# Optimization experiments

Hardware: AMD Instinct MI355X
Metric: run time of the kernel (lower is better)

## Reference

```python
import jax, jax.numpy as jnp
import numpy as np

B, N, F_IN, F_OUT = 8, 2048, 256, 256
H, D = 8, 32
LN_EPS = 1e-5


def setup_inputs() -> dict:
    key = jax.random.key(0)
    ks = jax.random.split(key, 8)
    s = 1.0 / np.sqrt(F_IN)
    so = 1.0 / np.sqrt(H * D)
    return {
        "x": jax.random.normal(ks[0], (B, N, F_IN), dtype=jnp.float32),
        "adj": jax.random.randint(ks[1], (B, N, N), 0, 2, dtype=jnp.int32),
        "Wq": jax.random.uniform(ks[2], (F_IN, H * D), jnp.float32, -s, s),
        "bq": jnp.zeros((H * D,), jnp.float32),
        "Wk": jax.random.uniform(ks[3], (F_IN, H * D), jnp.float32, -s, s),
        "bk": jnp.zeros((H * D,), jnp.float32),
        "Wv": jax.random.uniform(ks[4], (F_IN, H * D), jnp.float32, -s, s),
        "bv": jnp.zeros((H * D,), jnp.float32),
        "Wo": jax.random.uniform(ks[5], (H * D, F_OUT), jnp.float32, -so, so),
        "bo": jnp.zeros((F_OUT,), jnp.float32),
        "gamma": jnp.ones((F_OUT,), jnp.float32),
        "beta": jnp.zeros((F_OUT,), jnp.float32),
    }


def reference(x, adj, Wq, bq, Wk, bk, Wv, bv, Wo, bo, gamma, beta):
    b, n, _ = x.shape
    # QKV projections -> [B, H, N, D]
    q = (x @ Wq + bq).reshape(b, n, H, D).transpose(0, 2, 1, 3)
    k = (x @ Wk + bk).reshape(b, n, H, D).transpose(0, 2, 1, 3)
    v = (x @ Wv + bv).reshape(b, n, H, D).transpose(0, 2, 1, 3)
    # masked attention scores [B, H, N, N]
    scores = jnp.einsum('bhqd,bhkd->bhqk', q, k) / np.sqrt(D).astype(np.float32)
    scores = jnp.where(adj[:, None, :, :] == 0, -jnp.inf, scores)
    attn = jax.nn.softmax(scores, axis=-1)
    # dropout layers are identity in eval mode
    out = jnp.einsum('bhqk,bhkd->bhqd', attn, v)
    out = out.transpose(0, 2, 1, 3).reshape(b, n, H * D)
    out = out @ Wo + bo
    # LayerNorm
    mu = out.mean(-1, keepdims=True)
    var = out.var(-1, keepdims=True)
    out = (out - mu) * jax.lax.rsqrt(var + LN_EPS) * gamma + beta
    return out, attn.mean(axis=1)
```

## Files before the change

### kernel.cpp

```cpp
#include <hip/hip_runtime.h>


typedef __attribute__((ext_vector_type(8))) short short8;
typedef __attribute__((ext_vector_type(4))) float f32x4;
typedef __attribute__((ext_vector_type(4))) unsigned short us4;
typedef unsigned short u16;
typedef unsigned int u32;

#define SC2 0.25503486127240555f

__device__ __forceinline__ u16 cvt(float f) {
  __bf16 h = (__bf16)f;
  union { __bf16 h; u16 u; } v; v.h = h; return v.u;
}

__global__ __launch_bounds__(256) void k_prep(
    const int* __restrict__ adj, u32* __restrict__ packed,
    const float* __restrict__ w0, const float* __restrict__ w1,
    const float* __restrict__ w2, const float* __restrict__ w3,
    u16* __restrict__ o0, u16* __restrict__ o1,
    u16* __restrict__ o2, u16* __restrict__ o3) {
  int bid = blockIdx.x;
  if (bid < 256) {
    int z = bid >> 6, rem = bid & 63;
    const float* in; u16* out;
    if (z == 0) { in = w0; out = o0; }
    else if (z == 1) { in = w1; out = o1; }
    else if (z == 2) { in = w2; out = o2; }
    else { in = w3; out = o3; }
    __shared__ u16 t[32][33];
    int tx = threadIdx.x & 31, ty = threadIdx.x >> 5;
    int x0 = (rem & 7) * 32, y0 = (rem >> 3) * 32;
    for (int j = 0; j < 32; j += 8)
      t[ty + j][tx] = cvt(in[(y0 + ty + j) * 256 + x0 + tx]);
    __syncthreads();
    for (int j = 0; j < 32; j += 8)
      out[(x0 + ty + j) * 256 + y0 + tx] = t[tx][ty + j];
  } else {
    int lane = threadIdx.x & 63;
#pragma unroll 4
    for (int it = 0; it < 64; it++) {
      unsigned int i = ((bid - 256) * 64u + it) * 256u + threadIdx.x;
      unsigned long long m = __ballot(adj[i] != 0);
      if (lane == 0)       packed[i >> 5] = (u32)m;
      else if (lane == 32) packed[i >> 5] = (u32)(m >> 32);
    }
  }
}

__global__ __launch_bounds__(256) void k_qkv(
    const float* __restrict__ x, const u16* __restrict__ wt,
    const float* __restrict__ bq, const float* __restrict__ bk,
    const float* __restrict__ bv,
    u16* __restrict__ qw, u16* __restrict__ kw, u16* __restrict__ vt) {
  int l = threadIdx.x & 63, w = threadIdx.x >> 6;
  int lr = l & 15, lg = l >> 4;
  int row0 = blockIdx.y * 64 + w * 16;
  int c0 = blockIdx.x * 64;
  f32x4 acc[4] = {};
  const float* xr = x + (size_t)(row0 + lr) * 256 + lg * 8;
  const u16* wr = wt + (c0 + lr) * 256 + lg * 8;
  for (int k0 = 0; k0 < 256; k0 += 32) {
    f32x4 f0 = *(const f32x4*)(xr + k0);
    f32x4 f1 = *(const f32x4*)(xr + k0 + 4);
    short8 a;
    a[0] = (short)cvt(f0[0]); a[1] = (short)cvt(f0[1]);
    a[2] = (short)cvt(f0[2]); a[3] = (short)cvt(f0[3]);
    a[4] = (short)cvt(f1[0]); a[5] = (short)cvt(f1[1]);
    a[6] = (short)cvt(f1[2]); a[7] = (short)cvt(f1[3]);
#pragma unroll
    for (int ct = 0; ct < 4; ct++) {
      short8 bb = *(const short8*)(wr + ct * 16 * 256 + k0);
      acc[ct] = __builtin_amdgcn_mfma_f32_16x16x32_bf16(a, bb, acc[ct], 0, 0, 0);
    }
  }
  int mtx = blockIdx.x >> 2;
  const float* bias = (mtx == 0) ? bq : ((mtx == 1) ? bk : bv);
  int b = row0 >> 11, nbase = row0 & 2047;
#pragma unroll
  for (int ct = 0; ct < 4; ct++) {
    int cc = (c0 + ct * 16 + lr) & 255;
    int h = cc >> 5, d = cc & 31;
    float bs = bias[cc];
    if (mtx < 2) {
      u16* dst = (mtx == 0) ? qw : kw;
      float sc = (mtx == 0) ? SC2 : 1.0f;
#pragma unroll
      for (int rr = 0; rr < 4; rr++) {
        int n = nbase + lg * 4 + rr;
        dst[((b * 8 + h) * 2048 + n) * 32 + d] = cvt((acc[ct][rr] + bs) * sc);
      }
    } else {
      us4 pk;
#pragma unroll
      for (int rr = 0; rr < 4; rr++) pk[rr] = cvt(acc[ct][rr] + bs);
      *(us4*)(vt + (size_t)((b * 8 + h) * 32 + d) * 2048 + nbase + lg * 4) = pk;
    }
  }
}

__global__ __launch_bounds__(512) void k_attn(
    const u16* __restrict__ qw, const u16* __restrict__ kw,
    const u16* __restrict__ vt, const u32* __restrict__ packed,
    u16* __restrict__ ao, float* __restrict__ out2) {
  __shared__ __align__(16) u16 P[8][2048];
  __shared__ float lsbuf[8][32];
  int l = threadIdx.x & 63, wv = threadIdx.x >> 6;
  int lr = l & 15, lg = l >> 4;
  int b = blockIdx.y, q0 = blockIdx.x * 32;
  const u32* pkb = packed + (size_t)(b * 2048 + q0) * 64;

  {
    int h = wv;
    const u16* qb = qw + (size_t)((b * 8 + h) * 2048 + q0) * 32;
    const u16* kb = kw + (size_t)((b * 8 + h) * 2048) * 32;
    const u16* vb = vt + (size_t)((b * 8 + h) * 32) * 2048;
    short8 qf0 = *(const short8*)(qb + lr * 32 + lg * 8);
    short8 qf1 = *(const short8*)(qb + (16 + lr) * 32 + lg * 8);
    u16* Pt = &P[h][0];
    float ls0 = 0.f, ls1 = 0.f;
    f32x4 acc[2][2] = {};
    for (int ch = 0; ch < 32; ch++) {
      uint2 m0 = *(const uint2*)(pkb + lr * 64 + ch * 2);
      uint2 m1 = *(const uint2*)(pkb + (16 + lr) * 64 + ch * 2);
#pragma unroll
      for (int j = 0; j < 4; j++) {
        short8 kf = *(const short8*)(kb + (size_t)(ch * 64 + j * 16 + lr) * 32 + lg * 8);
        f32x4 z = {};
        f32x4 s0 = __builtin_amdgcn_mfma_f32_16x16x32_bf16(kf, qf0, z, 0, 0, 0);
        f32x4 s1 = __builtin_amdgcn_mfma_f32_16x16x32_bf16(kf, qf1, z, 0, 0, 0);
        u32 w0 = ((j & 2) ? m0.y : m0.x) >> ((j & 1) * 16 + lg * 4);
        u32 w1 = ((j & 2) ? m1.y : m1.x) >> ((j & 1) * 16 + lg * 4);
        us4 p0, p1;
#pragma unroll
        for (int rr = 0; rr < 4; rr++) {
          float e0 = __builtin_exp2f(s0[rr]);
          float e1 = __builtin_exp2f(s1[rr]);
          float em0 = ((w0 >> rr) & 1u) ? e0 : 0.0f;
          float em1 = ((w1 >> rr) & 1u) ? e1 : 0.0f;
          ls0 += em0; ls1 += em1;
          p0[rr] = cvt(em0); p1[rr] = cvt(em1);
        }
        int slot = 2 * j + (lg >> 1), offs = (lg & 1) * 4;
        *(us4*)(Pt + lr * 64 + ((slot ^ (lr & 7)) << 3) + offs) = p0;
        *(us4*)(Pt + (16 + lr) * 64 + ((slot ^ (lr & 7)) << 3) + offs) = p1;
      }
#pragma unroll
      for (int k2 = 0; k2 < 2; k2++) {
        short8 pa0 = *(const short8*)(Pt + lr * 64 +
                        (((k2 * 4 + lg) ^ (lr & 7)) << 3));
        short8 pa1 = *(const short8*)(Pt + (16 + lr) * 64 +
                        (((k2 * 4 + lg) ^ (lr & 7)) << 3));
#pragma unroll
        for (int dt = 0; dt < 2; dt++) {
          short8 vf = *(const short8*)(vb + (size_t)(dt * 16 + lr) * 2048 +
                                       ch * 64 + k2 * 32 + lg * 8);
          acc[0][dt] = __builtin_amdgcn_mfma_f32_16x16x32_bf16(pa0, vf, acc[0][dt], 0, 0, 0);
          acc[1][dt] = __builtin_amdgcn_mfma_f32_16x16x32_bf16(pa1, vf, acc[1][dt], 0, 0, 0);
        }
      }
    }
    ls0 += __shfl_xor(ls0, 16); ls0 += __shfl_xor(ls0, 32);
    ls1 += __shfl_xor(ls1, 16); ls1 += __shfl_xor(ls1, 32);
    ls0 = fmaxf(ls0, 1e-30f); ls1 = fmaxf(ls1, 1e-30f);
    if (l < 16) { lsbuf[h][lr] = ls0; lsbuf[h][16 + lr] = ls1; }
    float r0 = 1.0f / ls0, r1 = 1.0f / ls1;
#pragma unroll
    for (int qs = 0; qs < 2; qs++)
#pragma unroll
      for (int rr = 0; rr < 4; rr++) {
        float rq = __shfl(qs == 0 ? r0 : r1, lg * 4 + rr);
#pragma unroll
        for (int dt = 0; dt < 2; dt++) {
          int n = q0 + qs * 16 + lg * 4 + rr;
          ao[(size_t)(b * 2048 + n) * 256 + h * 32 + dt * 16 + lr] =
              cvt(acc[qs][dt][rr] * rq);
        }
      }
  }
  __syncthreads();

  {
    int qh = (wv >> 2) * 16;
    int c0 = (wv & 3) * 8;
    short8 qfh[8];
    float lil[8];
#pragma unroll
    for (int hh = 0; hh < 8; hh++) {
      qfh[hh] = *(const short8*)(qw +
          (size_t)((b * 8 + hh) * 2048 + q0 + qh + lr) * 32 + lg * 8);
      lil[hh] = -__log2f(lsbuf[hh][qh + lr]);
    }
    const u32* pkb2 = packed + (size_t)(b * 2048 + q0 + qh) * 64;
    for (int ch = c0; ch < c0 + 8; ch++) {
      uint2 mw = *(const uint2*)(pkb2 + lr * 64 + ch * 2);
#pragma unroll
      for (int j = 0; j < 4; j++) {
        f32x4 macc = {};
#pragma unroll
        for (int hh = 0; hh < 8; hh++) {
          const u16* kbh = kw + (size_t)((b * 8 + hh) * 2048) * 32;
          short8 kf = *(const short8*)(kbh +
              (size_t)(ch * 64 + j * 16 + lr) * 32 + lg * 8);
          f32x4 z = {};
          f32x4 s = __builtin_amdgcn_mfma_f32_16x16x32_bf16(kf, qfh[hh], z, 0, 0, 0);
#pragma unroll
          for (int rr = 0; rr < 4; rr++)
            macc[rr] += __builtin_exp2f(s[rr] + lil[hh]);
        }
        u32 wj = ((j & 2) ? mw.y : mw.x) >> ((j & 1) * 16 + lg * 4);
        f32x4 o;
#pragma unroll
        for (int rr = 0; rr < 4; rr++)
          o[rr] = ((wj >> rr) & 1u) ? macc[rr] * 0.125f : 0.0f;
        *(f32x4*)(out2 + (size_t)(b * 2048 + q0 + qh + lr) * 2048 +
                  ch * 64 + j * 16 + lg * 4) = o;
      }
    }
  }
}

__global__ __launch_bounds__(256) void k_oproj(
    const u16* __restrict__ ao, const u16* __restrict__ wto,
    const float* __restrict__ bo, const float* __restrict__ gamma,
    const float* __restrict__ beta, float* __restrict__ out) {
  int l = threadIdx.x & 63, w = threadIdx.x >> 6;
  int lr = l & 15, lg = l >> 4;
  int row0 = blockIdx.x * 64 + w * 16;
  f32x4 acc[16] = {};
  const u16* ar = ao + (size_t)(row0 + lr) * 256 + lg * 8;
  const u16* wr = wto + lr * 256 + lg * 8;
  for (int k0 = 0; k0 < 256; k0 += 32) {
    short8 a = *(const short8*)(ar + k0);
#pragma unroll
    for (int ct = 0; ct < 16; ct++) {
      short8 bb = *(const short8*)(wr + ct * 16 * 256 + k0);
      acc[ct] = __builtin_amdgcn_mfma_f32_16x16x32_bf16(a, bb, acc[ct], 0, 0, 0);
    }
  }
  float sum[4] = {0, 0, 0, 0}, sq[4] = {0, 0, 0, 0};
#pragma unroll
  for (int ct = 0; ct < 16; ct++) {
    float bs = bo[ct * 16 + lr];
#pragma unroll
    for (int rr = 0; rr < 4; rr++) {
      float v = acc[ct][rr] + bs;
      acc[ct][rr] = v;
      sum[rr] += v; sq[rr] += v * v;
    }
  }
#pragma unroll
  for (int rr = 0; rr < 4; rr++) {
    float s = sum[rr], q = sq[rr];
    s += __shfl_xor(s, 1); s += __shfl_xor(s, 2);
    s += __shfl_xor(s, 4); s += __shfl_xor(s, 8);
    q += __shfl_xor(q, 1); q += __shfl_xor(q, 2);
    q += __shfl_xor(q, 4); q += __shfl_xor(q, 8);
    float mu = s * (1.0f / 256.0f);
    float var = fmaxf(q * (1.0f / 256.0f) - mu * mu, 0.0f);
    sum[rr] = mu;
    sq[rr] = rsqrtf(var + 1e-5f);
  }
#pragma unroll
  for (int ct = 0; ct < 16; ct++) {
    float g = gamma[ct * 16 + lr], be = beta[ct * 16 + lr];
#pragma unroll
    for (int rr = 0; rr < 4; rr++) {
      int n = row0 + lg * 4 + rr;
      out[(size_t)n * 256 + ct * 16 + lr] =
          ((acc[ct][rr] - sum[rr]) * sq[rr]) * g + be;
    }
  }
}

extern "C" void kernel_launch(void* const* d_in, const int* in_sizes, int n_in,
                              void* d_out, int out_size, void* d_ws, size_t ws_size,
                              hipStream_t stream) {
  const float* x    = (const float*)d_in[0];
  const int*   adj  = (const int*)d_in[1];
  const float* Wq   = (const float*)d_in[2];
  const float* bq   = (const float*)d_in[3];
  const float* Wk   = (const float*)d_in[4];
  const float* bk   = (const float*)d_in[5];
  const float* Wv   = (const float*)d_in[6];
  const float* bv   = (const float*)d_in[7];
  const float* Wo   = (const float*)d_in[8];
  const float* bo   = (const float*)d_in[9];
  const float* gamma= (const float*)d_in[10];
  const float* beta = (const float*)d_in[11];

  char* ws = (char*)d_ws;
  u16* wtq = (u16*)(ws + 0);
  u16* wtk = (u16*)(ws + 131072);
  u16* wtv = (u16*)(ws + 262144);
  u16* wto = (u16*)(ws + 393216);
  u16* qw  = (u16*)(ws + 524288);
  u16* kw  = (u16*)(ws + 8912896);
  u16* vt  = (u16*)(ws + 17301504);
  u16* ao  = (u16*)(ws + 25690112);
  u32* pk  = (u32*)(ws + 34078720);

  float* out  = (float*)d_out;
  float* out2 = out + (size_t)8 * 2048 * 256;

  k_prep<<<dim3(2304), dim3(256), 0, stream>>>(adj, pk, Wq, Wk, Wv, Wo,
                                               wtq, wtk, wtv, wto);
  k_qkv<<<dim3(12, 256), dim3(256), 0, stream>>>(x, wtq, bq, bk, bv, qw, kw, vt);
  k_attn<<<dim3(64, 8), dim3(512), 0, stream>>>(qw, kw, vt, pk, ao, out2);
  k_oproj<<<dim3(256), dim3(256), 0, stream>>>(ao, wto, bo, gamma, beta, out);
}
```

Before: 377.0 us.

## Split attention kernel into per-head PV pass and separate head-mean probability pass

The fused attention kernel is split into two kernels. The first computes each (batch, head, 16-query) tile's PV output and writes reciprocal row sums to a workspace buffer. The second recomputes the scores to produce the head-averaged attention map, multiplying by the stored reciprocal with an fma instead of adding a log2 term inside exp2. Smaller 256-thread blocks with a 6-wave occupancy hint, and 2048 blocks per kernel, aim to raise occupancy and parallelism over the original 512-block grid. The cost is an extra launch, a global round-trip for the row sums, and less Q-fragment reuse per wave.

```diff
diff --git a/kernel.cpp b/kernel.cpp
--- a/kernel.cpp
+++ b/kernel.cpp
@@ -99,123 +99,110 @@
   }
 }
 
-__global__ __launch_bounds__(512) void k_attn(
+__global__ __launch_bounds__(256, 6) void k_attnA(
     const u16* __restrict__ qw, const u16* __restrict__ kw,
     const u16* __restrict__ vt, const u32* __restrict__ packed,
-    u16* __restrict__ ao, float* __restrict__ out2) {
-  __shared__ __align__(16) u16 P[8][2048];
-  __shared__ float lsbuf[8][32];
+    u16* __restrict__ ao, float* __restrict__ rlsb) {
+  __shared__ __align__(16) u16 P[4][1024];
   int l = threadIdx.x & 63, wv = threadIdx.x >> 6;
   int lr = l & 15, lg = l >> 4;
-  int b = blockIdx.y, q0 = blockIdx.x * 32;
+  int wid = blockIdx.x * 4 + wv;
+  int b = wid >> 10, h = (wid >> 7) & 7, q0 = (wid & 127) * 16;
+  const u16* qb = qw + (size_t)((b * 8 + h) * 2048 + q0) * 32;
+  const u16* kb = kw + (size_t)((b * 8 + h) * 2048) * 32;
+  const u16* vb = vt + (size_t)((b * 8 + h) * 32) * 2048;
+  short8 qf = *(const short8*)(qb + lr * 32 + lg * 8);
   const u32* pkb = packed + (size_t)(b * 2048 + q0) * 64;
-
-  {
-    int h = wv;
-    const u16* qb = qw + (size_t)((b * 8 + h) * 2048 + q0) * 32;
-    const u16* kb = kw + (size_t)((b * 8 + h) * 2048) * 32;
-    const u16* vb = vt + (size_t)((b * 8 + h) * 32) * 2048;
-    short8 qf0 = *(const short8*)(qb + lr * 32 + lg * 8);
-    short8 qf1 = *(const short8*)(qb + (16 + lr) * 32 + lg * 8);
-    u16* Pt = &P[h][0];
-    float ls0 = 0.f, ls1 = 0.f;
-    f32x4 acc[2][2] = {};
-    for (int ch = 0; ch < 32; ch++) {
-      uint2 m0 = *(const uint2*)(pkb + lr * 64 + ch * 2);
-      uint2 m1 = *(const uint2*)(pkb + (16 + lr) * 64 + ch * 2);
-#pragma unroll
-      for (int j = 0; j < 4; j++) {
-        short8 kf = *(const short8*)(kb + (size_t)(ch * 64 + j * 16 + lr) * 32 + lg * 8);
+  u16* Pt = &P[wv][0];
+  float ls = 0.f;
+  f32x4 acc[2] = {};
+  for (int ch = 0; ch < 32; ch++) {
+    uint2 m = *(const uint2*)(pkb + lr * 64 + ch * 2);
+#pragma unroll
+    for (int j = 0; j < 4; j++) {
+      short8 kf = *(const short8*)(kb + (size_t)(ch * 64 + j * 16 + lr) * 32 + lg * 8);
+      f32x4 z = {};
+      f32x4 s = __builtin_amdgcn_mfma_f32_16x16x32_bf16(kf, qf, z, 0, 0, 0);
+      u32 w = ((j & 2) ? m.y : m.x) >> ((j & 1) * 16 + lg * 4);
+      us4 p;
+#pragma unroll
+      for (int rr = 0; rr < 4; rr++) {
+        float e = __builtin_exp2f(s[rr]);
+        float em = ((w >> rr) & 1u) ? e : 0.0f;
+        ls += em;
+        p[rr] = cvt(em);
+      }
+      int slot = 2 * j + (lg >> 1), offs = (lg & 1) * 4;
+      *(us4*)(Pt + lr * 64 + ((slot ^ (lr & 7)) << 3) + offs) = p;
+    }
+#pragma unroll
+    for (int k2 = 0; k2 < 2; k2++) {
+      short8 pa = *(const short8*)(Pt + lr * 64 +
+                      (((k2 * 4 + lg) ^ (lr & 7)) << 3));
+#pragma unroll
+      for (int dt = 0; dt < 2; dt++) {
+        short8 vf = *(const short8*)(vb + (size_t)(dt * 16 + lr) * 2048 +
+                                     ch * 64 + k2 * 32 + lg * 8);
+        acc[dt] = __builtin_amdgcn_mfma_f32_16x16x32_bf16(pa, vf, acc[dt], 0, 0, 0);
+      }
+    }
+  }
+  ls += __shfl_xor(ls, 16); ls += __shfl_xor(ls, 32);
+  float rls = 1.0f / fmaxf(ls, 1e-30f);
+  if (l < 16) rlsb[(size_t)(b * 8 + h) * 2048 + q0 + lr] = rls;
+#pragma unroll
+  for (int rr = 0; rr < 4; rr++) {
+    float rq = __shfl(rls, lg * 4 + rr);
+#pragma unroll
+    for (int dt = 0; dt < 2; dt++) {
+      int n = q0 + lg * 4 + rr;
+      ao[(size_t)(b * 2048 + n) * 256 + h * 32 + dt * 16 + lr] =
+          cvt(acc[dt][rr] * rq);
+    }
+  }
+}
+
+__global__ __launch_bounds__(256, 6) void k_attnB(
+    const u16* __restrict__ qw, const u16* __restrict__ kw,
+    const u32* __restrict__ packed, const float* __restrict__ rlsb,
+    float* __restrict__ out2) {
+  int l = threadIdx.x & 63, wv = threadIdx.x >> 6;
+  int lr = l & 15, lg = l >> 4;
+  int wid = blockIdx.x * 4 + wv;
+  int b = wid >> 10, k8 = (wid >> 7) & 7, q0 = (wid & 127) * 16;
+  int c0 = k8 * 4;
+  short8 qfh[8];
+  float rls[8];
+#pragma unroll
+  for (int hh = 0; hh < 8; hh++) {
+    qfh[hh] = *(const short8*)(qw +
+        (size_t)((b * 8 + hh) * 2048 + q0 + lr) * 32 + lg * 8);
+    rls[hh] = rlsb[(size_t)(b * 8 + hh) * 2048 + q0 + lr];
+  }
+  const u32* pkb = packed + (size_t)(b * 2048 + q0) * 64;
+  const u16* kwb = kw + (size_t)(b * 8) * 2048 * 32;
+  for (int ch = c0; ch < c0 + 4; ch++) {
+    uint2 mw = *(const uint2*)(pkb + lr * 64 + ch * 2);
+#pragma unroll
+    for (int j = 0; j < 4; j++) {
+      f32x4 macc = {};
+#pragma unroll
+      for (int hh = 0; hh < 8; hh++) {
+        short8 kf = *(const short8*)(kwb + (size_t)hh * 2048 * 32 +
+            (size_t)(ch * 64 + j * 16 + lr) * 32 + lg * 8);
         f32x4 z = {};
-        f32x4 s0 = __builtin_amdgcn_mfma_f32_16x16x32_bf16(kf, qf0, z, 0, 0, 0);
-        f32x4 s1 = __builtin_amdgcn_mfma_f32_16x16x32_bf16(kf, qf1, z, 0, 0, 0);
-        u32 w0 = ((j & 2) ? m0.y : m0.x) >> ((j & 1) * 16 + lg * 4);
-        u32 w1 = ((j & 2) ? m1.y : m1.x) >> ((j & 1) * 16 + lg * 4);
-        us4 p0, p1;
-#pragma unroll
-        for (int rr = 0; rr < 4; rr++) {
-          float e0 = __builtin_exp2f(s0[rr]);
-          float e1 = __builtin_exp2f(s1[rr]);
-          float em0 = ((w0 >> rr) & 1u) ? e0 : 0.0f;
-          float em1 = ((w1 >> rr) & 1u) ? e1 : 0.0f;
-          ls0 += em0; ls1 += em1;
-          p0[rr] = cvt(em0); p1[rr] = cvt(em1);
-        }
-        int slot = 2 * j + (lg >> 1), offs = (lg & 1) * 4;
-        *(us4*)(Pt + lr * 64 + ((slot ^ (lr & 7)) << 3) + offs) = p0;
-        *(us4*)(Pt + (16 + lr) * 64 + ((slot ^ (lr & 7)) << 3) + offs) = p1;
+        f32x4 s = __builtin_amdgcn_mfma_f32_16x16x32_bf16(kf, qfh[hh], z, 0, 0, 0);
+#pragma unroll
+        for (int rr = 0; rr < 4; rr++)
+          macc[rr] = fmaf(__builtin_exp2f(s[rr]), rls[hh], macc[rr]);
       }
-#pragma unroll
-      for (int k2 = 0; k2 < 2; k2++) {
-        short8 pa0 = *(const short8*)(Pt + lr * 64 +
-                        (((k2 * 4 + lg) ^ (lr & 7)) << 3));
-        short8 pa1 = *(const short8*)(Pt + (16 + lr) * 64 +
-                        (((k2 * 4 + lg) ^ (lr & 7)) << 3));
-#pragma unroll
-        for (int dt = 0; dt < 2; dt++) {
-          short8 vf = *(const short8*)(vb + (size_t)(dt * 16 + lr) * 2048 +
-                                       ch * 64 + k2 * 32 + lg * 8);
-          acc[0][dt] = __builtin_amdgcn_mfma_f32_16x16x32_bf16(pa0, vf, acc[0][dt], 0, 0, 0);
-          acc[1][dt] = __builtin_amdgcn_mfma_f32_16x16x32_bf16(pa1, vf, acc[1][dt], 0, 0, 0);
-        }
-      }
-    }
-    ls0 += __shfl_xor(ls0, 16); ls0 += __shfl_xor(ls0, 32);
-    ls1 += __shfl_xor(ls1, 16); ls1 += __shfl_xor(ls1, 32);
-    ls0 = fmaxf(ls0, 1e-30f); ls1 = fmaxf(ls1, 1e-30f);
-    if (l < 16) { lsbuf[h][lr] = ls0; lsbuf[h][16 + lr] = ls1; }
-    float r0 = 1.0f / ls0, r1 = 1.0f / ls1;
-#pragma unroll
-    for (int qs = 0; qs < 2; qs++)
-#pragma unroll
-      for (int rr = 0; rr < 4; rr++) {
-        float rq = __shfl(qs == 0 ? r0 : r1, lg * 4 + rr);
-#pragma unroll
-        for (int dt = 0; dt < 2; dt++) {
-          int n = q0 + qs * 16 + lg * 4 + rr;
-          ao[(size_t)(b * 2048 + n) * 256 + h * 32 + dt * 16 + lr] =
-              cvt(acc[qs][dt][rr] * rq);
-        }
-      }
-  }
-  __syncthreads();
-
-  {
-    int qh = (wv >> 2) * 16;
-    int c0 = (wv & 3) * 8;
-    short8 qfh[8];
-    float lil[8];
-#pragma unroll
-    for (int hh = 0; hh < 8; hh++) {
-      qfh[hh] = *(const short8*)(qw +
-          (size_t)((b * 8 + hh) * 2048 + q0 + qh + lr) * 32 + lg * 8);
-      lil[hh] = -__log2f(lsbuf[hh][qh + lr]);
-    }
-    const u32* pkb2 = packed + (size_t)(b * 2048 + q0 + qh) * 64;
-    for (int ch = c0; ch < c0 + 8; ch++) {
-      uint2 mw = *(const uint2*)(pkb2 + lr * 64 + ch * 2);
-#pragma unroll
-      for (int j = 0; j < 4; j++) {
-        f32x4 macc = {};
-#pragma unroll
-        for (int hh = 0; hh < 8; hh++) {
-          const u16* kbh = kw + (size_t)((b * 8 + hh) * 2048) * 32;
-          short8 kf = *(const short8*)(kbh +
-              (size_t)(ch * 64 + j * 16 + lr) * 32 + lg * 8);
-          f32x4 z = {};
-          f32x4 s = __builtin_amdgcn_mfma_f32_16x16x32_bf16(kf, qfh[hh], z, 0, 0, 0);
-#pragma unroll
-          for (int rr = 0; rr < 4; rr++)
-            macc[rr] += __builtin_exp2f(s[rr] + lil[hh]);
-        }
-        u32 wj = ((j & 2) ? mw.y : mw.x) >> ((j & 1) * 16 + lg * 4);
-        f32x4 o;
-#pragma unroll
-        for (int rr = 0; rr < 4; rr++)
-          o[rr] = ((wj >> rr) & 1u) ? macc[rr] * 0.125f : 0.0f;
-        *(f32x4*)(out2 + (size_t)(b * 2048 + q0 + qh + lr) * 2048 +
-                  ch * 64 + j * 16 + lg * 4) = o;
-      }
+      u32 wj = ((j & 2) ? mw.y : mw.x) >> ((j & 1) * 16 + lg * 4);
+      f32x4 o;
+#pragma unroll
+      for (int rr = 0; rr < 4; rr++)
+        o[rr] = ((wj >> rr) & 1u) ? macc[rr] * 0.125f : 0.0f;
+      *(f32x4*)(out2 + (size_t)(b * 2048 + q0 + lr) * 2048 +
+                ch * 64 + j * 16 + lg * 4) = o;
     }
   }
 }
@@ -299,6 +286,7 @@
   u16* vt  = (u16*)(ws + 17301504);
   u16* ao  = (u16*)(ws + 25690112);
   u32* pk  = (u32*)(ws + 34078720);
+  float* rlsb = (float*)(ws + 38273024);
 
   float* out  = (float*)d_out;
   float* out2 = out + (size_t)8 * 2048 * 256;
@@ -306,6 +294,7 @@
   k_prep<<<dim3(2304), dim3(256), 0, stream>>>(adj, pk, Wq, Wk, Wv, Wo,
                                                wtq, wtk, wtv, wto);
   k_qkv<<<dim3(12, 256), dim3(256), 0, stream>>>(x, wtq, bq, bk, bv, qw, kw, vt);
-  k_attn<<<dim3(64, 8), dim3(512), 0, stream>>>(qw, kw, vt, pk, ao, out2);
+  k_attnA<<<dim3(2048), dim3(256), 0, stream>>>(qw, kw, vt, pk, ao, rlsb);
+  k_attnB<<<dim3(2048), dim3(256), 0, stream>>>(qw, kw, pk, rlsb, out2);
   k_oproj<<<dim3(256), dim3(256), 0, stream>>>(ao, wto, bo, gamma, beta, out);
 }
```

After: 593.1 us. 1.57x slower.
